# Performance work log

Hardware: AMD Instinct MI355X
Metric: run time of the kernel (lower is better)

The kernel has to match this reference:

```python
import jax, jax.numpy as jnp
import numpy as np

IN_C, H1, H2, FC1, NCLS = 16, 32, 64, 128, 10
N_NODES, N_EDGES = 20000, 100000


def _glorot(key, shape):
    fan_in, fan_out = shape[0], shape[-1]
    s = jnp.sqrt(6.0 / (fan_in + fan_out))
    return jax.random.uniform(key, shape, jnp.float32, -s, s)


def setup_inputs() -> dict:
    key = jax.random.key(0)
    ks = jax.random.split(key, 20)
    x = jax.random.normal(ks[0], (N_NODES, IN_C), jnp.float32)
    edge_index = jax.random.randint(ks[1], (2, N_EDGES), 0, N_NODES, jnp.int64)
    edge_attr = jax.random.uniform(ks[2], (N_EDGES, 1), jnp.float32)
    return {
        "x": x,
        "edge_index": edge_index,
        "edge_attr": edge_attr,
        # conv1 edge-MLP: 1 -> 25 -> IN_C*H1
        "w1a": _glorot(ks[3], (1, 25)), "b1a": jnp.zeros((25,), jnp.float32),
        "w1b": _glorot(ks[4], (25, IN_C * H1)), "b1b": jnp.zeros((IN_C * H1,), jnp.float32),
        "wr1": _glorot(ks[5], (IN_C, H1)), "bias1": jnp.zeros((H1,), jnp.float32),
        # conv2 edge-MLP: 1 -> 25 -> H1*H2 (=2048)
        "w2a": _glorot(ks[6], (1, 25)), "b2a": jnp.zeros((25,), jnp.float32),
        "w2b": _glorot(ks[7], (25, H1 * H2)), "b2b": jnp.zeros((H1 * H2,), jnp.float32),
        "wr2": _glorot(ks[8], (H1, H2)), "bias2": jnp.zeros((H2,), jnp.float32),
        # trailing FCs
        "fc1_w": _glorot(ks[9], (H2, FC1)), "fc1_b": jnp.zeros((FC1,), jnp.float32),
        "fc2_w": _glorot(ks[10], (FC1, NCLS)), "fc2_b": jnp.zeros((NCLS,), jnp.float32),
    }


def _nnconv(x, src, tgt, edge_attr, wa, ba, wb, bb, wroot, bias, in_c, out_c):
    # per-edge MLP-generated weight matrix [E, in_c, out_c]
    h = jax.nn.relu(edge_attr @ wa + ba) @ wb + bb
    W = h.reshape(-1, in_c, out_c)
    # gather source feats, per-edge matmul, scatter-max to targets
    msg = jnp.einsum("ei,eio->eo", x[src], W)  # [E, out_c]
    agg = jax.ops.segment_max(msg, tgt, num_segments=x.shape[0])
    agg = jnp.where(jnp.isfinite(agg), agg, 0.0)  # nodes with no in-edges -> 0 (PyG behavior)
    return agg + x @ wroot + bias


def reference(x, edge_index, edge_attr,
              w1a, b1a, w1b, b1b, wr1, bias1,
              w2a, b2a, w2b, b2b, wr2, bias2,
              fc1_w, fc1_b, fc2_w, fc2_b):
    src, tgt = edge_index[0], edge_index[1]
    h = jax.nn.elu(_nnconv(x, src, tgt, edge_attr, w1a, b1a, w1b, b1b, wr1, bias1, IN_C, H1))
    h = jax.nn.elu(_nnconv(h, src, tgt, edge_attr, w2a, b2a, w2b, b2b, wr2, bias2, H1, H2))
    h = jax.nn.elu(h @ fc1_w + fc1_b)
    h = h @ fc2_w + fc2_b
    return jax.nn.log_softmax(h, axis=1)
```

## Files before the change

### kernel.cpp

```cpp
#include <hip/hip_runtime.h>
#include <float.h>
#include <math.h>


#define NCONST 25
#define CH1 32
#define CH2 16
#define PACK_MASK 0x1FFFF

__device__ __forceinline__ void atomicMaxFloat(float* addr, float val) {
    if (val >= 0.f) atomicMax((int*)addr, __float_as_int(val));
    else            atomicMin((unsigned int*)addr, __float_as_uint(val));
}
__device__ __forceinline__ float readlane_f(float v, int l) {
    return __int_as_float(__builtin_amdgcn_readlane(__float_as_int(v), l));
}

__global__ void fill_kernel(float* agg, int nAgg, int* ords, int nOrd, int* hist, int nH) {
    int i = blockIdx.x * blockDim.x + threadIdx.x;
    int stride = gridDim.x * blockDim.x;
    int total = nAgg + nOrd + nH;
    for (; i < total; i += stride) {
        if (i < nAgg) agg[i] = -FLT_MAX;
        else if (i < nAgg + nOrd) ords[i - nAgg] = -1;
        else hist[i - nAgg - nOrd] = 0;
    }
}

__global__ void assign_hist_kernel(const float* __restrict__ ea,
                                   const float* __restrict__ w1a, const float* __restrict__ b1a,
                                   const float* __restrict__ w2a, const float* __restrict__ b2a,
                                   int E, int* __restrict__ segpack, int* __restrict__ hist) {
    __shared__ float t1[NCONST], t2[NCONST];
    __shared__ int lh[64];
    int tid = threadIdx.x;
    if (tid < NCONST) {
        float w = w1a[tid]; t1[tid] = (w != 0.f) ? (-b1a[tid] / w) : INFINITY;
        float v = w2a[tid]; t2[tid] = (v != 0.f) ? (-b2a[tid] / v) : INFINITY;
    }
    if (tid < 64) lh[tid] = 0;
    __syncthreads();
    int e = blockIdx.x * blockDim.x + tid;
    bool valid = e < E;
    if (valid) {
        float a = ea[e];
        int j1 = 0, j2 = 0;
        for (int k = 0; k < NCONST; ++k) { j1 += (t1[k] < a); j2 += (t2[k] < a); }
        segpack[e] = j1 | (j2 << 8);
        atomicAdd(&lh[j1], 1); atomicAdd(&lh[32 + j2], 1);
    }
    __syncthreads();
    if (tid < 64 && lh[tid]) atomicAdd(&hist[tid], lh[tid]);
}

__global__ void scanpad_kernel(const int* __restrict__ hist, int* __restrict__ cur) {
    __shared__ int h[64];
    int tid = threadIdx.x;
    h[tid] = hist[tid];
    __syncthreads();
    if (tid == 0) {
        int off = 0;
        for (int j = 0; j < 26; ++j) { cur[j] = off; off += ((h[j] + CH1 - 1) / CH1) * CH1; }
    } else if (tid == 1) {
        int off = 0;
        for (int j = 0; j < 26; ++j) { cur[32 + j] = off; off += ((h[32 + j] + CH2 - 1) / CH2) * CH2; }
    }
}

__global__ void scatter_kernel(const int* __restrict__ segpack, int E, int* __restrict__ cur,
                               int* __restrict__ order1, int* __restrict__ order2) {
    __shared__ int lh[64], lb[64];
    int tid = threadIdx.x;
    if (tid < 64) lh[tid] = 0;
    __syncthreads();
    int e = blockIdx.x * blockDim.x + tid;
    bool valid = e < E;
    int j1 = 0, j2 = 0, r1 = 0, r2 = 0;
    if (valid) {
        int p = segpack[e]; j1 = p & 0xFF; j2 = p >> 8;
        r1 = atomicAdd(&lh[j1], 1); r2 = atomicAdd(&lh[32 + j2], 1);
    }
    __syncthreads();
    if (tid < 64 && lh[tid]) lb[tid] = atomicAdd(&cur[tid], lh[tid]);
    __syncthreads();
    if (valid) {
        order1[lb[j1] + r1] = (j1 << 17) | e;
        order2[lb[32 + j2] + r2] = (j2 << 17) | e;
    }
}

__global__ void build_uv_fused(const float* w1a, const float* b1a, const float* w1b, const float* b1b,
                               const float* w2a, const float* b2a, const float* w2b, const float* b2b,
                               float* U1, float* V1, float* U2, float* V2) {
    __shared__ float swa[NCONST], sba[NCONST], st[NCONST];
    __shared__ int sr[NCONST];
    __shared__ unsigned msk_sh;
    int seg = blockIdx.y;
    int bx = blockIdx.x;
    int conv = (bx < 2) ? 0 : 1;
    const float* wa = conv ? w2a : w1a;
    const float* ba = conv ? b2a : b1a;
    int tid = threadIdx.x;
    if (tid < NCONST) {
        float w = wa[tid], b = ba[tid];
        swa[tid] = w; sba[tid] = b;
        st[tid] = (w != 0.f) ? (-b / w) : INFINITY;
    }
    __syncthreads();
    if (tid < NCONST) {
        int rk = 0;
        for (int l = 0; l < NCONST; ++l) rk += (st[l] < st[tid]) ? 1 : 0;
        sr[tid] = rk;
    }
    __syncthreads();
    if (tid == 0) {
        unsigned m = 0;
        for (int k = 0; k < NCONST; ++k) {
            float w = swa[k];
            bool act = (w > 0.f) ? (seg > sr[k])
                     : (w < 0.f) ? (seg <= sr[k])
                                 : (sba[k] > 0.f);
            if (act) m |= (1u << k);
        }
        msk_sh = m;
    }
    __syncthreads();
    unsigned msk = msk_sh;
    if (conv == 0) {
        int idx = bx * 256 + tid;
        float u = 0.f, v = 0.f;
        for (int k = 0; k < NCONST; ++k)
            if (msk & (1u << k)) { float w = w1b[k * 512 + idx]; u = fmaf(swa[k], w, u); v = fmaf(sba[k], w, v); }
        v += b1b[idx];
        U1[seg * 512 + idx] = u; V1[seg * 512 + idx] = v;
    } else {
        int idx = (bx - 2) * 256 + tid;
        float u = 0.f, v = 0.f;
        for (int k = 0; k < NCONST; ++k)
            if (msk & (1u << k)) { float w = w2b[k * 2048 + idx]; u = fmaf(swa[k], w, u); v = fmaf(sba[k], w, v); }
        v += b2b[idx];
        U2[seg * 2048 + idx] = u; V2[seg * 2048 + idx] = v;
    }
}

__global__ void edge1_kernel(const float* __restrict__ xin, const int* __restrict__ src,
                             const int* __restrict__ tgt, const float* __restrict__ ea,
                             const int* __restrict__ order, int cap,
                             const float* __restrict__ U, const float* __restrict__ V,
                             float* __restrict__ agg) {
    int wid = (blockIdx.x * blockDim.x + threadIdx.x) >> 6;
    int lane = threadIdx.x & 63;
    int base = wid * CH1;
    if (base >= cap) return;
    int pk = order[base + (lane & (CH1 - 1))];
    int p0 = __builtin_amdgcn_readfirstlane(pk);
    if (p0 < 0) return;
    int seg = p0 >> 17;
    int ev = (pk < 0) ? 0 : (pk & PACK_MASK);
    int sv = src[ev], tv = tgt[ev];
    float av = ea[ev];
    int half = lane >> 5, c = lane & 31;
    float Ur[16], Vr[16];
    {
        const float* Us = U + seg * 512 + c;
        const float* Vs = V + seg * 512 + c;
#pragma unroll
        for (int i = 0; i < 16; ++i) { Ur[i] = Us[i * 32]; Vr[i] = Vs[i * 32]; }
    }
#pragma unroll
    for (int t = 0; t < CH1; t += 2) {
        int pA = __builtin_amdgcn_readlane(pk, t);
        int pB = __builtin_amdgcn_readlane(pk, t + 1);
        int sA = __builtin_amdgcn_readlane(sv, t);
        int sB = __builtin_amdgcn_readlane(sv, t + 1);
        int tA = __builtin_amdgcn_readlane(tv, t);
        int tB = __builtin_amdgcn_readlane(tv, t + 1);
        float aA = readlane_f(av, t);
        float aB = readlane_f(av, t + 1);
        const float* xA = xin + sA * 16;
        const float* xB = xin + sB * 16;
        float ah = half ? aB : aA;
        int   th = half ? tB : tA;
        int   ph = half ? pB : pA;
        float acc = 0.f;
#pragma unroll
        for (int i = 0; i < 16; ++i) {
            float xi = half ? xB[i] : xA[i];
            acc = fmaf(xi, fmaf(ah, Ur[i], Vr[i]), acc);
        }
        if (ph >= 0) atomicMaxFloat(&agg[th * 32 + c], acc);
    }
}

__global__ void edge2_kernel(const float* __restrict__ xin, const int* __restrict__ src,
                             const int* __restrict__ tgt, const float* __restrict__ ea,
                             const int* __restrict__ order, int cap,
                             const float* __restrict__ U, const float* __restrict__ V,
                             float* __restrict__ agg) {
    int wid = (blockIdx.x * blockDim.x + threadIdx.x) >> 6;
    int lane = threadIdx.x & 63;
    int base = wid * CH2;
    if (base >= cap) return;
    int pk = order[base + (lane & (CH2 - 1))];
    int p0 = __builtin_amdgcn_readfirstlane(pk);
    if (p0 < 0) return;
    int seg = p0 >> 17;
    int ev = (pk < 0) ? 0 : (pk & PACK_MASK);
    int sv = src[ev], tv = tgt[ev];
    float av = ea[ev];
    float Ur[32], Vr[32];
    {
        const float* Us = U + seg * 2048 + lane;
        const float* Vs = V + seg * 2048 + lane;
#pragma unroll
        for (int i = 0; i < 32; ++i) { Ur[i] = Us[i * 64]; Vr[i] = Vs[i * 64]; }
    }
#pragma unroll
    for (int t = 0; t < CH2; t += 2) {
        int pA = __builtin_amdgcn_readlane(pk, t);
        int pB = __builtin_amdgcn_readlane(pk, t + 1);
        int sA = __builtin_amdgcn_readlane(sv, t);
        int sB = __builtin_amdgcn_readlane(sv, t + 1);
        int tA = __builtin_amdgcn_readlane(tv, t);
        int tB = __builtin_amdgcn_readlane(tv, t + 1);
        float aA = readlane_f(av, t);
        float aB = readlane_f(av, t + 1);
        const float* xA = xin + sA * 32;
        const float* xB = xin + sB * 32;
        float accA = 0.f, accB = 0.f;
#pragma unroll
        for (int i = 0; i < 32; ++i) {
            accA = fmaf(xA[i], fmaf(aA, Ur[i], Vr[i]), accA);
            accB = fmaf(xB[i], fmaf(aB, Ur[i], Vr[i]), accB);
        }
        if (pA >= 0) atomicMaxFloat(&agg[tA * 64 + lane], accA);
        if (pB >= 0) atomicMaxFloat(&agg[tB * 64 + lane], accB);
    }
}

__global__ void node1_kernel(const float* __restrict__ xin, const float* __restrict__ agg,
                             const float* __restrict__ wroot, const float* __restrict__ bias,
                             float* __restrict__ out, int N) {
    int idx = blockIdx.x * blockDim.x + threadIdx.x;
    if (idx >= N * 32) return;
    int n = idx >> 5, c = idx & 31;
    float v = agg[idx];
    if (v == -FLT_MAX) v = 0.f;
    float acc = v + bias[c];
#pragma unroll
    for (int i = 0; i < 16; ++i) acc = fmaf(xin[n * 16 + i], wroot[i * 32 + c], acc);
    out[idx] = acc > 0.f ? acc : expm1f(acc);
}

__global__ void tail_kernel(const float* __restrict__ h1, const float* __restrict__ agg2,
                            const float* __restrict__ wr2, const float* __restrict__ bias2,
                            const float* __restrict__ fc1w, const float* __restrict__ fc1b,
                            const float* __restrict__ fc2w, const float* __restrict__ fc2b,
                            float* __restrict__ out) {
    __shared__ __align__(16) float h2sh[4][64];
    __shared__ __align__(16) float h3sh[4][128];
    int w = threadIdx.x >> 6, lane = threadIdx.x & 63;
    int n = blockIdx.x * 4 + w;
    float v = agg2[n * 64 + lane];
    if (v == -FLT_MAX) v = 0.f;
    float acc = v + bias2[lane];
    const float* xr = h1 + n * 32;
#pragma unroll
    for (int i = 0; i < 32; ++i) acc = fmaf(xr[i], wr2[i * 64 + lane], acc);
    h2sh[w][lane] = acc > 0.f ? acc : expm1f(acc);
    __syncthreads();
    const float4* h2v = (const float4*)h2sh[w];
#pragma unroll
    for (int r = 0; r < 2; ++r) {
        int o = lane + r * 64;
        float a1 = fc1b[o];
#pragma unroll
        for (int q = 0; q < 16; ++q) {
            float4 hv = h2v[q];
            a1 = fmaf(hv.x, fc1w[(q * 4 + 0) * 128 + o], a1);
            a1 = fmaf(hv.y, fc1w[(q * 4 + 1) * 128 + o], a1);
            a1 = fmaf(hv.z, fc1w[(q * 4 + 2) * 128 + o], a1);
            a1 = fmaf(hv.w, fc1w[(q * 4 + 3) * 128 + o], a1);
        }
        h3sh[w][o] = a1 > 0.f ? a1 : expm1f(a1);
    }
    __syncthreads();
    float logit = -FLT_MAX;
    const float4* h3v = (const float4*)h3sh[w];
    if (lane < 10) {
        float a2 = fc2b[lane];
#pragma unroll
        for (int q = 0; q < 32; ++q) {
            float4 hv = h3v[q];
            a2 = fmaf(hv.x, fc2w[(q * 4 + 0) * 10 + lane], a2);
            a2 = fmaf(hv.y, fc2w[(q * 4 + 1) * 10 + lane], a2);
            a2 = fmaf(hv.z, fc2w[(q * 4 + 2) * 10 + lane], a2);
            a2 = fmaf(hv.w, fc2w[(q * 4 + 3) * 10 + lane], a2);
        }
        logit = a2;
    }
    float mx = -FLT_MAX;
#pragma unroll
    for (int i = 0; i < 10; ++i) mx = fmaxf(mx, __shfl(logit, i, 64));
    float s = 0.f;
#pragma unroll
    for (int i = 0; i < 10; ++i) s += expf(__shfl(logit, i, 64) - mx);
    if (lane < 10) out[n * 10 + lane] = logit - mx - logf(s);
}

extern "C" void kernel_launch(void* const* d_in, const int* in_sizes, int n_in,
                              void* d_out, int out_size, void* d_ws, size_t ws_size,
                              hipStream_t stream) {
    const float* x     = (const float*)d_in[0];
    const int*   eidx  = (const int*)d_in[1];
    const float* ea    = (const float*)d_in[2];
    const float* w1a   = (const float*)d_in[3];
    const float* b1a   = (const float*)d_in[4];
    const float* w1b   = (const float*)d_in[5];
    const float* b1b   = (const float*)d_in[6];
    const float* wr1   = (const float*)d_in[7];
    const float* bias1 = (const float*)d_in[8];
    const float* w2a   = (const float*)d_in[9];
    const float* b2a   = (const float*)d_in[10];
    const float* w2b   = (const float*)d_in[11];
    const float* b2b   = (const float*)d_in[12];
    const float* wr2   = (const float*)d_in[13];
    const float* bias2 = (const float*)d_in[14];
    const float* fc1w  = (const float*)d_in[15];
    const float* fc1b  = (const float*)d_in[16];
    const float* fc2w  = (const float*)d_in[17];
    const float* fc2b  = (const float*)d_in[18];

    const int N = in_sizes[0] / 16;
    const int E = in_sizes[2];
    const int* src = eidx;
    const int* tgt = eidx + E;

    const int cap1 = ((E + 26 * (CH1 - 1)) + CH1 - 1) / CH1 * CH1;
    const int cap2 = ((E + 26 * (CH2 - 1)) + CH2 - 1) / CH2 * CH2;

    float* ws = (float*)d_ws;
    size_t off = 0;
    int*      hist = (int*)(ws + off);      off += 64;
    int*      cur  = (int*)(ws + off);      off += 64;
    int*      segp = (int*)(ws + off);      off += E;
    int*      ord1 = (int*)(ws + off);      off += cap1;
    int*      ord2 = (int*)(ws + off);      off += cap2;
    float*    U1   = ws + off;              off += 26 * 512;
    float*    V1   = ws + off;              off += 26 * 512;
    float*    U2   = ws + off;              off += 26 * 2048;
    float*    V2   = ws + off;              off += 26 * 2048;
    float*    AGG1 = ws + off;              off += (size_t)N * 32;
    float*    AGG2 = ws + off;              off += (size_t)N * 64;
    float*    H1b  = ws + off;              off += (size_t)N * 32;

    fill_kernel<<<512, 256, 0, stream>>>(AGG1, N * 96, ord1, cap1 + cap2, hist, 64);
    assign_hist_kernel<<<(E + 255) / 256, 256, 0, stream>>>(ea, w1a, b1a, w2a, b2a, E, segp, hist);
    scanpad_kernel<<<1, 64, 0, stream>>>(hist, cur);
    scatter_kernel<<<(E + 255) / 256, 256, 0, stream>>>(segp, E, cur, ord1, ord2);
    build_uv_fused<<<dim3(10, 26), 256, 0, stream>>>(w1a, b1a, w1b, b1b, w2a, b2a, w2b, b2b,
                                                     U1, V1, U2, V2);
    {
        int waves = cap1 / CH1;
        edge1_kernel<<<(waves + 3) / 4, 256, 0, stream>>>(x, src, tgt, ea, ord1, cap1, U1, V1, AGG1);
    }
    node1_kernel<<<(N * 32 + 255) / 256, 256, 0, stream>>>(x, AGG1, wr1, bias1, H1b, N);
    {
        int waves = cap2 / CH2;
        edge2_kernel<<<(waves + 3) / 4, 256, 0, stream>>>(H1b, src, tgt, ea, ord2, cap2, U2, V2, AGG2);
    }
    tail_kernel<<<N / 4, 256, 0, stream>>>(H1b, AGG2, wr2, bias2, fc1w, fc1b, fc2w, fc2b, (float*)d_out);
}
```

Baseline: 231.1 us.

## Split fused tail into node2/fc1/fc2 kernels and add launch bounds

The fused tail kernel, which used shared memory and syncthreads, is split into three separate kernels (node2, fc1, fc2) that pass intermediate activations through new global workspace buffers. The edge kernels gain __launch_bounds__ hints and switch their U/V register arrays to ext_vector types, aiming for better register allocation and occupancy. The split removes block-level syncs and shared-memory traffic but adds global round trips for the N×64 and N×128 intermediates and two extra launches.

```diff
diff --git a/kernel.cpp b/kernel.cpp
--- a/kernel.cpp
+++ b/kernel.cpp
@@ -7,6 +7,9 @@
 #define CH1 32
 #define CH2 16
 #define PACK_MASK 0x1FFFF
+
+typedef float vf16 __attribute__((ext_vector_type(16)));
+typedef float vf32 __attribute__((ext_vector_type(32)));
 
 __device__ __forceinline__ void atomicMaxFloat(float* addr, float val) {
     if (val >= 0.f) atomicMax((int*)addr, __float_as_int(val));
@@ -143,11 +146,12 @@
     }
 }
 
-__global__ void edge1_kernel(const float* __restrict__ xin, const int* __restrict__ src,
-                             const int* __restrict__ tgt, const float* __restrict__ ea,
-                             const int* __restrict__ order, int cap,
-                             const float* __restrict__ U, const float* __restrict__ V,
-                             float* __restrict__ agg) {
+__global__ void __launch_bounds__(256, 4)
+edge1_kernel(const float* __restrict__ xin, const int* __restrict__ src,
+             const int* __restrict__ tgt, const float* __restrict__ ea,
+             const int* __restrict__ order, int cap,
+             const float* __restrict__ U, const float* __restrict__ V,
+             float* __restrict__ agg) {
     int wid = (blockIdx.x * blockDim.x + threadIdx.x) >> 6;
     int lane = threadIdx.x & 63;
     int base = wid * CH1;
@@ -160,7 +164,7 @@
     int sv = src[ev], tv = tgt[ev];
     float av = ea[ev];
     int half = lane >> 5, c = lane & 31;
-    float Ur[16], Vr[16];
+    vf16 Ur, Vr;
     {
         const float* Us = U + seg * 512 + c;
         const float* Vs = V + seg * 512 + c;
@@ -192,11 +196,12 @@
     }
 }
 
-__global__ void edge2_kernel(const float* __restrict__ xin, const int* __restrict__ src,
-                             const int* __restrict__ tgt, const float* __restrict__ ea,
-                             const int* __restrict__ order, int cap,
-                             const float* __restrict__ U, const float* __restrict__ V,
-                             float* __restrict__ agg) {
+__global__ void __launch_bounds__(256, 2)
+edge2_kernel(const float* __restrict__ xin, const int* __restrict__ src,
+             const int* __restrict__ tgt, const float* __restrict__ ea,
+             const int* __restrict__ order, int cap,
+             const float* __restrict__ U, const float* __restrict__ V,
+             float* __restrict__ agg) {
     int wid = (blockIdx.x * blockDim.x + threadIdx.x) >> 6;
     int lane = threadIdx.x & 63;
     int base = wid * CH2;
@@ -208,7 +213,7 @@
     int ev = (pk < 0) ? 0 : (pk & PACK_MASK);
     int sv = src[ev], tv = tgt[ev];
     float av = ea[ev];
-    float Ur[32], Vr[32];
+    vf32 Ur, Vr;
     {
         const float* Us = U + seg * 2048 + lane;
         const float* Vs = V + seg * 2048 + lane;
@@ -252,52 +257,42 @@
     out[idx] = acc > 0.f ? acc : expm1f(acc);
 }
 
-__global__ void tail_kernel(const float* __restrict__ h1, const float* __restrict__ agg2,
-                            const float* __restrict__ wr2, const float* __restrict__ bias2,
-                            const float* __restrict__ fc1w, const float* __restrict__ fc1b,
-                            const float* __restrict__ fc2w, const float* __restrict__ fc2b,
-                            float* __restrict__ out) {
-    __shared__ __align__(16) float h2sh[4][64];
-    __shared__ __align__(16) float h3sh[4][128];
-    int w = threadIdx.x >> 6, lane = threadIdx.x & 63;
-    int n = blockIdx.x * 4 + w;
-    float v = agg2[n * 64 + lane];
+__global__ void node2_kernel(const float* __restrict__ h1, const float* __restrict__ agg,
+                             const float* __restrict__ wroot, const float* __restrict__ bias,
+                             float* __restrict__ out, int N) {
+    int idx = blockIdx.x * blockDim.x + threadIdx.x;
+    if (idx >= N * 64) return;
+    int n = idx >> 6, c = idx & 63;
+    float v = agg[idx];
     if (v == -FLT_MAX) v = 0.f;
-    float acc = v + bias2[lane];
-    const float* xr = h1 + n * 32;
-#pragma unroll
-    for (int i = 0; i < 32; ++i) acc = fmaf(xr[i], wr2[i * 64 + lane], acc);
-    h2sh[w][lane] = acc > 0.f ? acc : expm1f(acc);
-    __syncthreads();
-    const float4* h2v = (const float4*)h2sh[w];
-#pragma unroll
-    for (int r = 0; r < 2; ++r) {
-        int o = lane + r * 64;
-        float a1 = fc1b[o];
-#pragma unroll
-        for (int q = 0; q < 16; ++q) {
-            float4 hv = h2v[q];
-            a1 = fmaf(hv.x, fc1w[(q * 4 + 0) * 128 + o], a1);
-            a1 = fmaf(hv.y, fc1w[(q * 4 + 1) * 128 + o], a1);
-            a1 = fmaf(hv.z, fc1w[(q * 4 + 2) * 128 + o], a1);
-            a1 = fmaf(hv.w, fc1w[(q * 4 + 3) * 128 + o], a1);
-        }
-        h3sh[w][o] = a1 > 0.f ? a1 : expm1f(a1);
-    }
-    __syncthreads();
+    float acc = v + bias[c];
+#pragma unroll
+    for (int i = 0; i < 32; ++i) acc = fmaf(h1[n * 32 + i], wroot[i * 64 + c], acc);
+    out[idx] = acc > 0.f ? acc : expm1f(acc);
+}
+
+__global__ void fc1_kernel(const float* __restrict__ h2, const float* __restrict__ w,
+                           const float* __restrict__ b, float* __restrict__ out, int N) {
+    int idx = blockIdx.x * blockDim.x + threadIdx.x;
+    if (idx >= N * 128) return;
+    int n = idx >> 7, c = idx & 127;
+    float acc = b[c];
+#pragma unroll
+    for (int i = 0; i < 64; ++i) acc = fmaf(h2[n * 64 + i], w[i * 128 + c], acc);
+    out[idx] = acc > 0.f ? acc : expm1f(acc);
+}
+
+__global__ void fc2_kernel(const float* __restrict__ h3, const float* __restrict__ w,
+                           const float* __restrict__ b, float* __restrict__ out, int N) {
+    int n = blockIdx.x * (blockDim.x / 64) + threadIdx.x / 64;
+    int o = threadIdx.x % 64;
+    if (n >= N) return;
     float logit = -FLT_MAX;
-    const float4* h3v = (const float4*)h3sh[w];
-    if (lane < 10) {
-        float a2 = fc2b[lane];
-#pragma unroll
-        for (int q = 0; q < 32; ++q) {
-            float4 hv = h3v[q];
-            a2 = fmaf(hv.x, fc2w[(q * 4 + 0) * 10 + lane], a2);
-            a2 = fmaf(hv.y, fc2w[(q * 4 + 1) * 10 + lane], a2);
-            a2 = fmaf(hv.z, fc2w[(q * 4 + 2) * 10 + lane], a2);
-            a2 = fmaf(hv.w, fc2w[(q * 4 + 3) * 10 + lane], a2);
-        }
-        logit = a2;
+    if (o < 10) {
+        float acc = b[o];
+#pragma unroll
+        for (int i = 0; i < 128; ++i) acc = fmaf(h3[n * 128 + i], w[i * 10 + o], acc);
+        logit = acc;
     }
     float mx = -FLT_MAX;
 #pragma unroll
@@ -305,7 +300,7 @@
     float s = 0.f;
 #pragma unroll
     for (int i = 0; i < 10; ++i) s += expf(__shfl(logit, i, 64) - mx);
-    if (lane < 10) out[n * 10 + lane] = logit - mx - logf(s);
+    if (o < 10) out[n * 10 + o] = logit - mx - logf(s);
 }
 
 extern "C" void kernel_launch(void* const* d_in, const int* in_sizes, int n_in,
@@ -353,6 +348,8 @@
     float*    AGG1 = ws + off;              off += (size_t)N * 32;
     float*    AGG2 = ws + off;              off += (size_t)N * 64;
     float*    H1b  = ws + off;              off += (size_t)N * 32;
+    float*    H2b  = ws + off;              off += (size_t)N * 64;
+    float*    H3b  = ws + off;              off += (size_t)N * 128;
 
     fill_kernel<<<512, 256, 0, stream>>>(AGG1, N * 96, ord1, cap1 + cap2, hist, 64);
     assign_hist_kernel<<<(E + 255) / 256, 256, 0, stream>>>(ea, w1a, b1a, w2a, b2a, E, segp, hist);
@@ -369,5 +366,7 @@
         int waves = cap2 / CH2;
         edge2_kernel<<<(waves + 3) / 4, 256, 0, stream>>>(H1b, src, tgt, ea, ord2, cap2, U2, V2, AGG2);
     }
-    tail_kernel<<<N / 4, 256, 0, stream>>>(H1b, AGG2, wr2, bias2, fc1w, fc1b, fc2w, fc2b, (float*)d_out);
-}
+    node2_kernel<<<(N * 64 + 255) / 256, 256, 0, stream>>>(H1b, AGG2, wr2, bias2, H2b, N);
+    fc1_kernel<<<(N * 128 + 255) / 256, 256, 0, stream>>>(H2b, fc1w, fc1b, H3b, N);
+    fc2_kernel<<<(N + 3) / 4, 256, 0, stream>>>(H3b, fc2w, fc2b, (float*)d_out, N);
+}
```

New measurement: 271.7 us. 17.6% more time.
